# Kernel tuning notes

Hardware: AMD Instinct MI355X
Metric: run time of the kernel (lower is better)

The kernel has to match this reference:

```python
import jax, jax.numpy as jnp
import numpy as np
import math

B, D, L, H, K, CONV_N = 32, 128, 1024, 8, 7, 4
DK = D // H
EPS = 1e-5


def make_pos_encoding():
    i = np.arange(D, dtype=np.float64)
    freqs = np.where(i % 2 == 0, 10000.0 ** (-i / D), -(10000.0 ** ((1 - i) / D)))
    phases = np.where(i % 2 == 0, 0.0, math.pi / 2)
    pos = np.arange(L, dtype=np.float64)[None, :]  # [1, L]
    pe = np.sin(pos * freqs[:, None] + phases[:, None])  # [D, L]
    return jnp.asarray(pe, dtype=jnp.float32)


def layer_norm_2d(x, w, b):
    # nn.LayerNorm([D, L]) on [B, D, L]: normalize jointly over last two dims
    mu = jnp.mean(x, axis=(1, 2), keepdims=True)
    var = jnp.var(x, axis=(1, 2), keepdims=True)
    return (x - mu) * jax.lax.rsqrt(var + EPS) * w[None] + b[None]


def setup_inputs():
    key = jax.random.key(0)
    ks = jax.random.split(key, 24)
    s = 0.05
    x = jax.random.normal(ks[0], (B, D, L), jnp.float32)
    lengths = jax.random.randint(ks[1], (B,), L // 2, L + 1)
    mask = (jnp.arange(L)[None, :] >= lengths[:, None]).astype(jnp.float32)  # 1 = pad
    inp = {
        "x": x,
        "mask": mask,
        "pos_enc": make_pos_encoding(),
        "normb_w": jnp.ones((D, L), jnp.float32),
        "normb_b": jnp.zeros((D, L), jnp.float32),
        "dw_w": jax.random.normal(ks[2], (CONV_N, D, K), jnp.float32) * s,
        "dw_b": jnp.zeros((CONV_N, D), jnp.float32),
        "pw_w": jax.random.normal(ks[3], (CONV_N, D, D), jnp.float32) * s,
        "pw_b": jnp.zeros((CONV_N, D), jnp.float32),
        "norms_w": jnp.ones((CONV_N, D, L), jnp.float32),
        "norms_b": jnp.zeros((CONV_N, D, L), jnp.float32),
        "qw": jax.random.normal(ks[4], (D, D), jnp.float32) * s,
        "qb": jnp.zeros((D,), jnp.float32),
        "kw": jax.random.normal(ks[5], (D, D), jnp.float32) * s,
        "kb": jnp.zeros((D,), jnp.float32),
        "vw": jax.random.normal(ks[6], (D, D), jnp.float32) * s,
        "vb": jnp.zeros((D,), jnp.float32),
        "aw": jax.random.normal(ks[7], (D, D), jnp.float32) * s,  # attention output fc
        "ab": jnp.zeros((D,), jnp.float32),
        "norme_w": jnp.ones((D, L), jnp.float32),
        "norme_b": jnp.zeros((D, L), jnp.float32),
        "fw": jax.random.normal(ks[8], (D, D), jnp.float32) * s,  # final fc
        "fb": jnp.zeros((D,), jnp.float32),
    }
    return inp


def reference(x, mask, pos_enc, normb_w, normb_b, dw_w, dw_b, pw_w, pw_b,
              norms_w, norms_b, qw, qb, kw, kb, vw, vb, aw, ab,
              norme_w, norme_b, fw, fb):
    # positional encoding + pre-LN
    out = x + pos_enc[None]
    res = out
    out = layer_norm_2d(out, normb_w, normb_b)

    # conv stack (eval mode: dropout is identity)
    for i in range(CONV_N):
        h = jax.lax.conv_general_dilated(
            out, dw_w[i][:, None, :],  # depthwise: [D, 1, K]
            window_strides=(1,), padding=[(K // 2, K // 2)],
            dimension_numbers=("NCH", "OIH", "NCH"),
            feature_group_count=D) + dw_b[i][None, :, None]
        h = jnp.einsum("bcl,oc->bol", h, pw_w[i]) + pw_b[i][None, :, None]
        out = jax.nn.relu(h) + res
        res = out
        out = layer_norm_2d(out, norms_w[i], norms_b[i])

    # multi-head self-attention (manual bmm-softmax-bmm, scale 1/sqrt(d_k))
    xt = jnp.swapaxes(out, 1, 2)  # [B, L, D]
    q = (xt @ qw.T + qb).reshape(B, L, H, DK)
    k = (xt @ kw.T + kb).reshape(B, L, H, DK)
    v = (xt @ vw.T + vb).reshape(B, L, H, DK)
    scores = jnp.einsum("bqhd,bkhd->bhqk", q, k) * (1.0 / math.sqrt(DK))
    m = mask[:, None, None, :]  # broadcast over heads and query dim
    scores = scores * (1.0 - m) + m * (-1e30)
    attn = jax.nn.softmax(scores, axis=-1)
    o = jnp.einsum("bhqk,bkhd->bqhd", attn, v).reshape(B, L, D)
    o = o @ aw.T + ab
    o = jnp.swapaxes(o, 1, 2)  # [B, D, L]

    out = o + res
    res = out
    out = layer_norm_2d(out, norme_w, norme_b)
    out = jnp.einsum("bdl,ed->bel", out, fw) + fb[None, :, None]
    out = jax.nn.relu(out) + res
    return out
```

## Files before the change

### kernel.cpp

```cpp
#include <hip/hip_runtime.h>

#define NB 32
#define ND 128
#define NL 1024
#define NDL (ND*NL)
#define STATS_B 16
#define STATS_R (32*STATS_B)

typedef __attribute__((ext_vector_type(8))) short bf16x8;
typedef __attribute__((ext_vector_type(4))) float f32x4;
typedef unsigned short u16;

__device__ __forceinline__ f32x4 mfma_bf16_16x16x32(bf16x8 a, bf16x8 b, f32x4 c) {
#if defined(__HIP_DEVICE_COMPILE__)
  return __builtin_amdgcn_mfma_f32_16x16x32_bf16(a, b, c, 0, 0, 0);
#else
  return c;
#endif
}

__device__ __forceinline__ float exp2fast(float x) {
#if defined(__HIP_DEVICE_COMPILE__) && __has_builtin(__builtin_amdgcn_exp2f)
  return __builtin_amdgcn_exp2f(x);
#elif defined(__HIP_DEVICE_COMPILE__)
  return __expf(x * 0.6931471805599453f);
#else
  return x;
#endif
}

__device__ __forceinline__ float bf2f(u16 u) {
  union { unsigned u; float f; } c; c.u = ((unsigned)u) << 16; return c.f;
}
__device__ __forceinline__ u16 bf16rnd(float f) {
  union { float f; unsigned u; } c; c.f = f;
  return (u16)((c.u + 0x7FFFu + ((c.u >> 16) & 1u)) >> 16);
}
__device__ __forceinline__ unsigned packpair(float a, float b) {
  return (unsigned)bf16rnd(a) | ((unsigned)bf16rnd(b) << 16);
}
__device__ __forceinline__ unsigned packtrunc(float a, float b) {
  unsigned ua = __float_as_uint(a), ub = __float_as_uint(b);
  return (ub & 0xFFFF0000u) | (ua >> 16);
}
__device__ __forceinline__ bf16x8 packbf8(float4 a, float4 b) {
  union { unsigned u[4]; bf16x8 v; } r;
  r.u[0] = packpair(a.x, a.y); r.u[1] = packpair(a.z, a.w);
  r.u[2] = packpair(b.x, b.y); r.u[3] = packpair(b.z, b.w);
  return r.v;
}

__device__ __forceinline__ void blockRedAtomic(float s, float sq, float* base) {
  __shared__ float red[32];
#pragma unroll
  for (int off = 32; off > 0; off >>= 1) {
    s  += __shfl_down(s, off, 64);
    sq += __shfl_down(sq, off, 64);
  }
  int wave = threadIdx.x >> 6;
  int nw = blockDim.x >> 6;
  if ((threadIdx.x & 63) == 0) { red[wave*2] = s; red[wave*2+1] = sq; }
  __syncthreads();
  if (threadIdx.x == 0) {
    float ts = 0.f, tq = 0.f;
    for (int i = 0; i < nw; ++i) { ts += red[i*2]; tq += red[i*2+1]; }
    unsafeAtomicAdd(base,     ts);
    unsafeAtomicAdd(base + 1, tq);
  }
}

__global__ void k_zero(float* stats) {
  int t = threadIdx.x;
#pragma unroll
  for (int i = 0; i < 3; ++i) stats[i*1024 + t] = 0.f;
}

__global__ __launch_bounds__(256) void k_len(const float* __restrict__ mask,
                                             int* __restrict__ lenbuf) {
  __shared__ int csh;
  int b = blockIdx.x, tid = threadIdx.x;
  if (tid == 0) csh = 0;
  __syncthreads();
  int cnt = 0;
  for (int i = tid; i < NL; i += 256) cnt += (mask[(size_t)b*NL + i] == 0.f) ? 1 : 0;
#pragma unroll
  for (int off = 32; off > 0; off >>= 1) cnt += __shfl_down(cnt, off, 64);
  if ((tid & 63) == 0) atomicAdd(&csh, cnt);
  __syncthreads();
  if (tid == 0) lenbuf[b] = csh;
}

__global__ __launch_bounds__(256) void k_addpos(const float* __restrict__ x,
                                                const float* __restrict__ pe,
                                                u16* __restrict__ res,
                                                float* __restrict__ stats0) {
  int b = blockIdx.x >> 6;
  int off = ((blockIdx.x & 63) << 11) + (threadIdx.x << 3);
  const float4* xp = (const float4*)(x + (size_t)b*NDL + off);
  const float4* pp = (const float4*)(pe + off);
  float s = 0.f, sq = 0.f;
  float rv[8];
#pragma unroll
  for (int i = 0; i < 2; ++i) {
    float4 a = xp[i], p = pp[i];
    rv[i*4+0] = a.x + p.x; rv[i*4+1] = a.y + p.y;
    rv[i*4+2] = a.z + p.z; rv[i*4+3] = a.w + p.w;
  }
#pragma unroll
  for (int j = 0; j < 8; ++j) { s += rv[j]; sq += rv[j]*rv[j]; }
  uint4 pk;
  pk.x = packpair(rv[0], rv[1]); pk.y = packpair(rv[2], rv[3]);
  pk.z = packpair(rv[4], rv[5]); pk.w = packpair(rv[6], rv[7]);
  *(uint4*)(res + (size_t)b*NDL + off) = pk;
  blockRedAtomic(s, sq, stats0 + b*STATS_B);
}


__device__ __forceinline__ void load_w_frags16(const float* __restrict__ W,
                                               int wo, int lo, int hi, bf16x8 af[4]) {
#pragma unroll
  for (int kk = 0; kk < 4; ++kk) {
    const float4* wp = (const float4*)(W + (size_t)(wo + lo)*128 + kk*32 + hi*8);
    af[kk] = packbf8(wp[0], wp[1]);
  }
}

__device__ __forceinline__ void mfma_core16(const unsigned* xs, bf16x8 af[4],
                                            int lo, int hi, f32x4 acc[4]) {
#pragma unroll
  for (int ln = 0; ln < 4; ++ln) {
#pragma unroll
    for (int kk = 0; kk < 4; ++kk) {
      int l = ln*16 + lo;
      int off = (l*256 + kk*64 + hi*16) ^ ((lo & 7) << 4);
      bf16x8 bf = *(const bf16x8*)((const char*)xs + off);
      acc[ln] = mfma_bf16_16x16x32(af[kk], bf, acc[ln]);
    }
  }
}

__device__ __forceinline__ void conv_row8(const u16* __restrict__ srow,
                                          const float* __restrict__ lwrow,
                                          const float* __restrict__ lbrow,
                                          int base, float mu, float rstd,
                                          const float* wk, float bias0,
                                          float* h ) {
  float wa[14];
  bool interior = (base >= 4) && (base + 12 <= NL);
  if (interior) {
    const uint2* sp = (const uint2*)(srow + base - 4);
    const float4* wp = (const float4*)(lwrow + base - 4);
    const float4* bp = (const float4*)(lbrow + base - 4);
#pragma unroll
    for (int qd = 0; qd < 4; ++qd) {
      uint2 sv2 = sp[qd];
      float4 w4 = wp[qd], b4 = bp[qd];
      float sv[4] = {bf2f((u16)(sv2.x & 0xFFFF)), bf2f((u16)(sv2.x >> 16)),
                     bf2f((u16)(sv2.y & 0xFFFF)), bf2f((u16)(sv2.y >> 16))};
      float wv[4] = {w4.x, w4.y, w4.z, w4.w};
      float bv[4] = {b4.x, b4.y, b4.z, b4.w};
#pragma unroll
      for (int e = 0; e < 4; ++e) {
        int j = qd*4 + e - 1;
        if (j >= 0 && j < 14)
          wa[j] = (sv[e] - mu)*rstd*wv[e] + bv[e];
      }
    }
  } else {
#pragma unroll
    for (int j = 0; j < 14; ++j) {
      int gl = base + j - 3;
      float v = 0.f;
      if (gl >= 0 && gl < NL)
        v = (bf2f(srow[gl]) - mu)*rstd*lwrow[gl] + lbrow[gl];
      wa[j] = v;
    }
  }
#pragma unroll
  for (int l = 0; l < 8; ++l) {
    float acc = bias0;
#pragma unroll
    for (int j = 0; j < 7; ++j) acc += wa[l+j]*wk[j];
    h[l] = acc;
  }
}

template<int MODE>
__global__ __launch_bounds__(512) void k_gemm_mfma(
    const u16* __restrict__ src16, const float* __restrict__ W,
    const float* __restrict__ bias,
    const u16* __restrict__ res16, u16* __restrict__ wr16,
    float* __restrict__ outf,
    const float* __restrict__ lnw, const float* __restrict__ lnb,
    const float* __restrict__ dww, const float* __restrict__ dwb,
    const float* __restrict__ statsIn, float* __restrict__ statsOut) {
  __shared__ unsigned xs[4096];
  int b  = blockIdx.x >> 4;
  int l0 = (blockIdx.x & 15) << 6;
  int tid = threadIdx.x;
  int wave = tid >> 6, lane = tid & 63;
  int lo = lane & 15, hi = lane >> 4;
  int wo = wave * 16;

  float mu = 0.f, rstd = 0.f;
  if (MODE == 0 || MODE == 3) {
    mu = statsIn[b*STATS_B] * (1.f/NDL);
    rstd = rsqrtf(statsIn[b*STATS_B + 1]*(1.f/NDL) - mu*mu + 1e-5f);
  }

  if (MODE == 0) {
    int c2 = tid >> 3, lq = tid & 7;
    int c = c2*2, base = l0 + lq*8;
    float wk0[7], wk1[7];
#pragma unroll
    for (int j = 0; j < 7; ++j) { wk0[j] = dww[c*7 + j]; wk1[j] = dww[(c+1)*7 + j]; }
    const u16* sa = src16 + (size_t)b*NDL + (size_t)c*NL;
    const float* la  = lnw + (size_t)c*NL;
    const float* lbv = lnb + (size_t)c*NL;
    float h0[8], h1[8];
    conv_row8(sa,      la,      lbv,      base, mu, rstd, wk0, dwb[c],   h0);
    conv_row8(sa + NL, la + NL, lbv + NL, base, mu, rstd, wk1, dwb[c+1], h1);
#pragma unroll
    for (int l = 0; l < 8; ++l) {
      int ll = lq*8 + l;
      xs[(ll << 6) | (c2 ^ ((ll & 7) << 2))] = packpair(h0[l], h1[l]);
    }
  } else if (MODE == 1) {
    for (int i = tid; i < 1024; i += 512) {
      int c2 = i >> 4, lq = (i & 15) << 2;
      int c = c2*2;
      const u16* sp = src16 + (size_t)b*NDL + (size_t)c*NL + l0 + lq;
      uint2 ra = *(const uint2*)sp;
      uint2 rb = *(const uint2*)(sp + NL);
      unsigned wv[4];
      wv[0] = (ra.x & 0xFFFFu) | (rb.x << 16);
      wv[1] = (ra.x >> 16)     | (rb.x & 0xFFFF0000u);
      wv[2] = (ra.y & 0xFFFFu) | (rb.y << 16);
      wv[3] = (ra.y >> 16)     | (rb.y & 0xFFFF0000u);
#pragma unroll
      for (int j = 0; j < 4; ++j) {
        int l = lq + j;
        xs[(l << 6) | (c2 ^ ((l & 7) << 2))] = wv[j];
      }
    }
  } else {
    for (int i = tid; i < 1024; i += 512) {
      int c2 = i >> 4, lq = (i & 15) << 2;
      int c = c2*2;
      const u16* sp = src16 + (size_t)b*NDL + (size_t)c*NL + l0 + lq;
      uint2 ra = *(const uint2*)sp;
      uint2 rb = *(const uint2*)(sp + NL);
      float sa[4] = {bf2f((u16)(ra.x & 0xFFFF)), bf2f((u16)(ra.x >> 16)),
                     bf2f((u16)(ra.y & 0xFFFF)), bf2f((u16)(ra.y >> 16))};
      float sb[4] = {bf2f((u16)(rb.x & 0xFFFF)), bf2f((u16)(rb.x >> 16)),
                     bf2f((u16)(rb.y & 0xFFFF)), bf2f((u16)(rb.y >> 16))};
      size_t gi = (size_t)c*NL + l0 + lq;
      float4 w0 = *(const float4*)(lnw + gi), w1 = *(const float4*)(lnw + gi + NL);
      float4 bb0 = *(const float4*)(lnb + gi), bb1 = *(const float4*)(lnb + gi + NL);
      float va[4] = {(sa[0]-mu)*rstd*w0.x + bb0.x, (sa[1]-mu)*rstd*w0.y + bb0.y,
                     (sa[2]-mu)*rstd*w0.z + bb0.z, (sa[3]-mu)*rstd*w0.w + bb0.w};
      float vb[4] = {(sb[0]-mu)*rstd*w1.x + bb1.x, (sb[1]-mu)*rstd*w1.y + bb1.y,
                     (sb[2]-mu)*rstd*w1.z + bb1.z, (sb[3]-mu)*rstd*w1.w + bb1.w};
#pragma unroll
      for (int j = 0; j < 4; ++j) {
        int l = lq + j;
        xs[(l << 6) | (c2 ^ ((l & 7) << 2))] = packpair(va[j], vb[j]);
      }
    }
  }

  u16 rpre[16];
#pragma unroll
  for (int ln = 0; ln < 4; ++ln)
#pragma unroll
    for (int r = 0; r < 4; ++r)
      rpre[ln*4+r] = res16[((size_t)b*ND + wo + hi*4 + r)*NL + l0 + ln*16 + lo];

  bf16x8 af[4];
  load_w_frags16(W, wo, lo, hi, af);
  f32x4 acc[4];
#pragma unroll
  for (int ln = 0; ln < 4; ++ln) acc[ln] = (f32x4){0.f,0.f,0.f,0.f};

  __syncthreads();
  mfma_core16(xs, af, lo, hi, acc);

  if (MODE == 0 || MODE == 1) {
    float s = 0.f, sq = 0.f;
#pragma unroll
    for (int ln = 0; ln < 4; ++ln) {
      int l = l0 + ln*16 + lo;
#pragma unroll
      for (int r = 0; r < 4; ++r) {
        int o = wo + hi*4 + r;
        size_t gi = ((size_t)b*ND + o)*NL + l;
        float v = acc[ln][r] + bias[o];
        if (MODE == 0) v = fmaxf(v, 0.f);
        v += bf2f(rpre[ln*4+r]);
        wr16[gi] = bf16rnd(v);
        s += v; sq += v*v;
      }
    }
    blockRedAtomic(s, sq, statsOut + b*STATS_B);
  } else {
#pragma unroll
    for (int ln = 0; ln < 4; ++ln) {
      int l = l0 + ln*16 + lo;
#pragma unroll
      for (int r = 0; r < 4; ++r) {
        int o = wo + hi*4 + r;
        size_t gi = ((size_t)b*ND + o)*NL + l;
        outf[gi] = fmaxf(acc[ln][r] + bias[o], 0.f) + bf2f(rpre[ln*4+r]);
      }
    }
  }
}

__global__ __launch_bounds__(512) void k_qkv_mfma(
    const u16* __restrict__ src16,
    const float* __restrict__ qw, const float* __restrict__ kw, const float* __restrict__ vw,
    const float* __restrict__ qb, const float* __restrict__ kb, const float* __restrict__ vb,
    u16* __restrict__ qo, u16* __restrict__ ko, u16* __restrict__ vo,
    const float* __restrict__ lnw, const float* __restrict__ lnb,
    const float* __restrict__ statsIn) {
  __shared__ unsigned xs[4096];
  int b  = blockIdx.x >> 4;
  int l0 = (blockIdx.x & 15) << 6;
  int tid = threadIdx.x;
  int wave = tid >> 6, lane = tid & 63;
  int lo = lane & 15, hi = lane >> 4;
  int wo = wave * 16;

  float mu = statsIn[b*STATS_B] * (1.f/NDL);
  float rstd = rsqrtf(statsIn[b*STATS_B + 1]*(1.f/NDL) - mu*mu + 1e-5f);
  for (int i = tid; i < 1024; i += 512) {
    int c2 = i >> 4, lq = (i & 15) << 2;
    int c = c2*2;
    const u16* sp = src16 + (size_t)b*NDL + (size_t)c*NL + l0 + lq;
    uint2 ra = *(const uint2*)sp;
    uint2 rb = *(const uint2*)(sp + NL);
    float sa[4] = {bf2f((u16)(ra.x & 0xFFFF)), bf2f((u16)(ra.x >> 16)),
                   bf2f((u16)(ra.y & 0xFFFF)), bf2f((u16)(ra.y >> 16))};
    float sb[4] = {bf2f((u16)(rb.x & 0xFFFF)), bf2f((u16)(rb.x >> 16)),
                   bf2f((u16)(rb.y & 0xFFFF)), bf2f((u16)(rb.y >> 16))};
    size_t gi = (size_t)c*NL + l0 + lq;
    float4 w0 = *(const float4*)(lnw + gi), w1 = *(const float4*)(lnw + gi + NL);
    float4 bb0 = *(const float4*)(lnb + gi), bb1 = *(const float4*)(lnb + gi + NL);
    float va[4] = {(sa[0]-mu)*rstd*w0.x + bb0.x, (sa[1]-mu)*rstd*w0.y + bb0.y,
                   (sa[2]-mu)*rstd*w0.z + bb0.z, (sa[3]-mu)*rstd*w0.w + bb0.w};
    float vb4[4] = {(sb[0]-mu)*rstd*w1.x + bb1.x, (sb[1]-mu)*rstd*w1.y + bb1.y,
                    (sb[2]-mu)*rstd*w1.z + bb1.z, (sb[3]-mu)*rstd*w1.w + bb1.w};
#pragma unroll
    for (int j = 0; j < 4; ++j) {
      int l = lq + j;
      xs[(l << 6) | (c2 ^ ((l & 7) << 2))] = packpair(va[j], vb4[j]);
    }
  }
  __syncthreads();

  const float* Ws[3] = {qw, kw, vw};
  const float* Bs[3] = {qb, kb, vb};
  u16* Os[3] = {qo, ko, vo};
#pragma unroll 1
  for (int mat = 0; mat < 3; ++mat) {
    bf16x8 af[4];
    load_w_frags16(Ws[mat], wo, lo, hi, af);
    f32x4 acc[4];
#pragma unroll
    for (int ln = 0; ln < 4; ++ln) acc[ln] = (f32x4){0.f,0.f,0.f,0.f};
    mfma_core16(xs, af, lo, hi, acc);
    float oscale = (mat == 0) ? 0.25f*1.4426950408889634f : 1.0f;
    const float* bias = Bs[mat];
    u16* op = Os[mat];
#pragma unroll
    for (int ln = 0; ln < 4; ++ln) {
      int l = l0 + ln*16 + lo;
      int o4 = wo + hi*4;
      float vx = (acc[ln][0] + bias[o4+0]) * oscale;
      float vy = (acc[ln][1] + bias[o4+1]) * oscale;
      float vz = (acc[ln][2] + bias[o4+2]) * oscale;
      float vw4 = (acc[ln][3] + bias[o4+3]) * oscale;
      uint2 pk; pk.x = packpair(vx, vy); pk.y = packpair(vz, vw4);
      *(uint2*)(op + ((size_t)b*NL + l)*ND + o4) = pk;
    }
  }
}

template<bool MASKED>
__device__ __forceinline__ void attn_tile(bf16x8 kf0, bf16x8 kf1, bf16x8 vf,
                                          bf16x8 onesf, const bf16x8 qf[4],
                                          f32x4 acc[4], f32x4 dacc[4],
                                          int kb, int len, int hi) {
#pragma unroll
  for (int qt = 0; qt < 4; ++qt) {
    f32x4 z = (f32x4){0.f,0.f,0.f,0.f};
    f32x4 s0 = mfma_bf16_16x16x32(kf0, qf[qt], z);
    f32x4 s1 = mfma_bf16_16x16x32(kf1, qf[qt], z);
    float e[8];
#pragma unroll
    for (int r = 0; r < 4; ++r) {
      float e0 = exp2fast(s0[r]);
      float e1 = exp2fast(s1[r]);
      if (MASKED) {
        e0 = (kb + hi*4 + r < len)      ? e0 : 0.f;
        e1 = (kb + 16 + hi*4 + r < len) ? e1 : 0.f;
      }
      e[r] = e0; e[r+4] = e1;
    }
    union { unsigned u[4]; bf16x8 v; } pu;
    pu.u[0] = packtrunc(e[0], e[1]);
    pu.u[1] = packtrunc(e[2], e[3]);
    pu.u[2] = packtrunc(e[4], e[5]);
    pu.u[3] = packtrunc(e[6], e[7]);
    acc[qt]  = mfma_bf16_16x16x32(vf,    pu.v, acc[qt]);
    dacc[qt] = mfma_bf16_16x16x32(onesf, pu.v, dacc[qt]);
  }
}

__device__ __forceinline__ bf16x8 ldKrow(const u16* kbase, int key, int hi) {
  union { uint4 u; bf16x8 v; } r;
  r.u = *(const uint4*)(kbase + (size_t)key*ND + hi*8);
  return r.v;
}

__global__ __launch_bounds__(512) void k_attn_fused(
    const u16* __restrict__ q, const u16* __restrict__ k,
    const u16* __restrict__ v, const int* __restrict__ lenbuf,
    u16* __restrict__ att_t) {
  __shared__ short kv[16384];
  int bid = blockIdx.x;
  int b  = bid >> 4;
  int h  = (bid >> 1) & 7;
  int qh = bid & 1;
  int tid = threadIdx.x;
  int len = lenbuf[b];
  int nkt = (len + 31) >> 5;
  int kstage = nkt << 5;

  for (int idx = tid; idx < 2048; idx += 512) {
    int keyp = idx >> 2, vq = idx & 3;
    int key = keyp*2;
    if (key >= kstage) break;
    int vlo = vq*4;
    uint2 ra, rb; ra.x = ra.y = rb.x = rb.y = 0u;
    size_t voff = ((size_t)b*NL + key)*ND + h*16 + vlo;
    if (key < len)     ra = *(const uint2*)(v + voff);
    if (key + 1 < len) rb = *(const uint2*)(v + voff + ND);
    unsigned wv[4];
    wv[0] = (ra.x & 0xFFFFu) | (rb.x << 16);
    wv[1] = (ra.x >> 16)     | (rb.x & 0xFFFF0000u);
    wv[2] = (ra.y & 0xFFFFu) | (rb.y << 16);
    wv[3] = (ra.y >> 16)     | (rb.y & 0xFFFF0000u);
    int kt = key >> 5, w = key & 31;
    int vhi, ii;
    if (w < 16) { vhi = w >> 2; ii = w & 3; }
    else        { vhi = (w - 16) >> 2; ii = 4 + (w & 3); }
#pragma unroll
    for (int e = 0; e < 4; ++e)
      *(unsigned*)(kv + kt*512 + (vhi*16 + vlo + e)*8 + ii) = wv[e];
  }
  __syncthreads();

  int wave = tid >> 6, lane = tid & 63;
  int lo = lane & 15, hi = lane >> 4;
  int q0 = qh*512 + wave*64;

  bf16x8 qf[4];
#pragma unroll
  for (int qt = 0; qt < 4; ++qt) {
    if (hi < 2) {
      union { uint4 u; bf16x8 v; } qu;
      qu.u = *(const uint4*)(q + ((size_t)b*NL + q0 + qt*16 + lo)*ND + h*16 + hi*8);
      qf[qt] = qu.v;
    } else {
      qf[qt] = (bf16x8){0,0,0,0,0,0,0,0};
    }
  }
  const short oneb = (short)0x3F80;
  bf16x8 onesf = (bf16x8){oneb,oneb,oneb,oneb,oneb,oneb,oneb,oneb};
  f32x4 acc[4], dacc[4];
#pragma unroll
  for (int qt = 0; qt < 4; ++qt) {
    acc[qt]  = (f32x4){0.f,0.f,0.f,0.f};
    dacc[qt] = (f32x4){0.f,0.f,0.f,0.f};
  }

  int fullt = len >> 5;
  const u16* kbase = k + (size_t)b*NL*ND + h*16;

  bf16x8 cka = (bf16x8){0,0,0,0,0,0,0,0}, ckb = cka, cv;
  if (hi < 2) {
    cka = ldKrow(kbase, lo, hi);
    ckb = ldKrow(kbase, 16 + lo, hi);
  }
  cv = *(const bf16x8*)(kv + lane*8);

  for (int kt = 0; kt < nkt; ++kt) {
    bf16x8 nka = cka, nkb = ckb, nv = cv;
    if (kt + 1 < nkt) {
      int kb2 = (kt+1)*32;
      if (hi < 2) {
        nka = ldKrow(kbase, kb2 + lo, hi);
        nkb = ldKrow(kbase, kb2 + 16 + lo, hi);
      }
      nv = *(const bf16x8*)(kv + (kt+1)*512 + lane*8);
    }
    if (kt < fullt) attn_tile<false>(cka, ckb, cv, onesf, qf, acc, dacc, kt*32, len, hi);
    else            attn_tile<true >(cka, ckb, cv, onesf, qf, acc, dacc, kt*32, len, hi);
    cka = nka; ckb = nkb; cv = nv;
  }
#pragma unroll
  for (int qt = 0; qt < 4; ++qt) {
    float inv = 1.f / dacc[qt][0];
    size_t obase = ((size_t)b*ND + h*16)*NL + q0 + qt*16 + lo;
#pragma unroll
    for (int r = 0; r < 4; ++r)
      att_t[obase + (size_t)(hi*4 + r)*NL] = bf16rnd(acc[qt][r] * inv);
  }
}

extern "C" void kernel_launch(void* const* d_in, const int* in_sizes, int n_in,
                              void* d_out, int out_size, void* d_ws, size_t ws_size,
                              hipStream_t stream) {
  (void)in_sizes; (void)n_in; (void)out_size; (void)ws_size;
  const float* x       = (const float*)d_in[0];
  const float* mask    = (const float*)d_in[1];
  const float* pe      = (const float*)d_in[2];
  const float* normb_w = (const float*)d_in[3];
  const float* normb_b = (const float*)d_in[4];
  const float* dw_w    = (const float*)d_in[5];
  const float* dw_b    = (const float*)d_in[6];
  const float* pw_w    = (const float*)d_in[7];
  const float* pw_b    = (const float*)d_in[8];
  const float* norms_w = (const float*)d_in[9];
  const float* norms_b = (const float*)d_in[10];
  const float* qw      = (const float*)d_in[11];
  const float* qb      = (const float*)d_in[12];
  const float* kw      = (const float*)d_in[13];
  const float* kb      = (const float*)d_in[14];
  const float* vw      = (const float*)d_in[15];
  const float* vb      = (const float*)d_in[16];
  const float* aw      = (const float*)d_in[17];
  const float* ab      = (const float*)d_in[18];
  const float* norme_w = (const float*)d_in[19];
  const float* norme_b = (const float*)d_in[20];
  const float* fw      = (const float*)d_in[21];
  const float* fb      = (const float*)d_in[22];

  float* out = (float*)d_out;
  float* ws  = (float*)d_ws;
  const size_t NT = (size_t)NB*ND*NL;
  u16* resA = (u16*)ws;
  u16* resB = (u16*)(ws + NT/2);
  u16* qb16 = (u16*)(ws + NT);
  u16* kb16 = (u16*)(ws + 3*NT/2);
  u16* vb16 = (u16*)(ws + 2*NT);
  float* stats = ws + 3*NT;
  int* lenbuf = (int*)(stats + 6*STATS_R);
  u16* att16 = resB;

  k_zero<<<dim3(1), dim3(1024), 0, stream>>>(stats);
  k_len<<<dim3(NB), dim3(256), 0, stream>>>(mask, lenbuf);
  k_addpos<<<dim3(2048), dim3(256), 0, stream>>>(x, pe, resA, stats);

  for (int i = 0; i < 4; ++i) {
    const float* lw = (i == 0) ? normb_w : norms_w + (size_t)(i-1)*NDL;
    const float* lb = (i == 0) ? normb_b : norms_b + (size_t)(i-1)*NDL;
    const u16* rsrc = (i & 1) ? resB : resA;
    u16*       rdst = (i & 1) ? resA : resB;
    k_gemm_mfma<0><<<dim3(NB*16), dim3(512), 0, stream>>>(
        rsrc, pw_w + i*ND*ND, pw_b + i*ND, rsrc, rdst, nullptr,
        lw, lb, dw_w + i*ND*7, dw_b + i*ND,
        stats + i*STATS_R, stats + (i+1)*STATS_R);
  }

  const float* ln3w = norms_w + (size_t)3*NDL;
  const float* ln3b = norms_b + (size_t)3*NDL;
  k_qkv_mfma<<<dim3(NB*16), dim3(512), 0, stream>>>(
      resA, qw, kw, vw, qb, kb, vb, qb16, kb16, vb16, ln3w, ln3b, stats + 4*STATS_R);

  k_attn_fused<<<dim3(NB*8*2), dim3(512), 0, stream>>>(qb16, kb16, vb16, lenbuf, att16);

  k_gemm_mfma<1><<<dim3(NB*16), dim3(512), 0, stream>>>(
      att16, aw, ab, resA, resA, nullptr, nullptr, nullptr, nullptr, nullptr,
      nullptr, stats + 5*STATS_R);
  k_gemm_mfma<3><<<dim3(NB*16), dim3(512), 0, stream>>>(
      resA, fw, fb, resA, nullptr, out, norme_w, norme_b, nullptr, nullptr,
      stats + 5*STATS_R, nullptr);
}
```

Baseline: 172.1 us.

## Double threads per GEMM block and split attention queries across more blocks

The GEMM and QKV kernels now launch 1024 threads per block. Each wave covers 32 of the 64 L columns instead of all 64, and each thread does one staging chunk and a 4-wide conv instead of 8. The attention kernel now uses four query quarters per (batch, head) with 32 queries per wave, doubling the block count. The goal is more waves in flight to hide latency. The cost is that each block reloads K/V into shared memory twice as often, there are more atomics in the stats reductions, and register pressure is tighter under the new launch bounds.

```diff
diff --git a/kernel.cpp b/kernel.cpp
--- a/kernel.cpp
+++ b/kernel.cpp
@@ -125,13 +125,13 @@
   }
 }
 
-__device__ __forceinline__ void mfma_core16(const unsigned* xs, bf16x8 af[4],
-                                            int lo, int hi, f32x4 acc[4]) {
-#pragma unroll
-  for (int ln = 0; ln < 4; ++ln) {
+__device__ __forceinline__ void mfma_core2(const unsigned* xs, bf16x8 af[4],
+                                           int lo, int hi, int loff, f32x4 acc[2]) {
+#pragma unroll
+  for (int ln = 0; ln < 2; ++ln) {
 #pragma unroll
     for (int kk = 0; kk < 4; ++kk) {
-      int l = ln*16 + lo;
+      int l = loff + ln*16 + lo;
       int off = (l*256 + kk*64 + hi*16) ^ ((lo & 7) << 4);
       bf16x8 bf = *(const bf16x8*)((const char*)xs + off);
       acc[ln] = mfma_bf16_16x16x32(af[kk], bf, acc[ln]);
@@ -139,20 +139,20 @@
   }
 }
 
-__device__ __forceinline__ void conv_row8(const u16* __restrict__ srow,
+__device__ __forceinline__ void conv_row4(const u16* __restrict__ srow,
                                           const float* __restrict__ lwrow,
                                           const float* __restrict__ lbrow,
                                           int base, float mu, float rstd,
                                           const float* wk, float bias0,
                                           float* h ) {
-  float wa[14];
-  bool interior = (base >= 4) && (base + 12 <= NL);
+  float wa[10];
+  bool interior = (base >= 4) && (base + 8 <= NL);
   if (interior) {
     const uint2* sp = (const uint2*)(srow + base - 4);
     const float4* wp = (const float4*)(lwrow + base - 4);
     const float4* bp = (const float4*)(lbrow + base - 4);
 #pragma unroll
-    for (int qd = 0; qd < 4; ++qd) {
+    for (int qd = 0; qd < 3; ++qd) {
       uint2 sv2 = sp[qd];
       float4 w4 = wp[qd], b4 = bp[qd];
       float sv[4] = {bf2f((u16)(sv2.x & 0xFFFF)), bf2f((u16)(sv2.x >> 16)),
@@ -162,13 +162,13 @@
 #pragma unroll
       for (int e = 0; e < 4; ++e) {
         int j = qd*4 + e - 1;
-        if (j >= 0 && j < 14)
+        if (j >= 0 && j < 10)
           wa[j] = (sv[e] - mu)*rstd*wv[e] + bv[e];
       }
     }
   } else {
 #pragma unroll
-    for (int j = 0; j < 14; ++j) {
+    for (int j = 0; j < 10; ++j) {
       int gl = base + j - 3;
       float v = 0.f;
       if (gl >= 0 && gl < NL)
@@ -177,7 +177,7 @@
     }
   }
 #pragma unroll
-  for (int l = 0; l < 8; ++l) {
+  for (int l = 0; l < 4; ++l) {
     float acc = bias0;
 #pragma unroll
     for (int j = 0; j < 7; ++j) acc += wa[l+j]*wk[j];
@@ -186,7 +186,7 @@
 }
 
 template<int MODE>
-__global__ __launch_bounds__(512) void k_gemm_mfma(
+__global__ __launch_bounds__(1024, 8) void k_gemm_mfma(
     const u16* __restrict__ src16, const float* __restrict__ W,
     const float* __restrict__ bias,
     const u16* __restrict__ res16, u16* __restrict__ wr16,
@@ -200,7 +200,8 @@
   int tid = threadIdx.x;
   int wave = tid >> 6, lane = tid & 63;
   int lo = lane & 15, hi = lane >> 4;
-  int wo = wave * 16;
+  int wo = (wave & 7) * 16;
+  int loff = (wave >> 3) * 32;
 
   float mu = 0.f, rstd = 0.f;
   if (MODE == 0 || MODE == 3) {
@@ -208,88 +209,81 @@
     rstd = rsqrtf(statsIn[b*STATS_B + 1]*(1.f/NDL) - mu*mu + 1e-5f);
   }
 
+  int c2 = tid >> 4, lq4 = (tid & 15) << 2;
+  int c = c2*2;
   if (MODE == 0) {
-    int c2 = tid >> 3, lq = tid & 7;
-    int c = c2*2, base = l0 + lq*8;
+    int base = l0 + lq4;
     float wk0[7], wk1[7];
 #pragma unroll
     for (int j = 0; j < 7; ++j) { wk0[j] = dww[c*7 + j]; wk1[j] = dww[(c+1)*7 + j]; }
     const u16* sa = src16 + (size_t)b*NDL + (size_t)c*NL;
     const float* la  = lnw + (size_t)c*NL;
     const float* lbv = lnb + (size_t)c*NL;
-    float h0[8], h1[8];
-    conv_row8(sa,      la,      lbv,      base, mu, rstd, wk0, dwb[c],   h0);
-    conv_row8(sa + NL, la + NL, lbv + NL, base, mu, rstd, wk1, dwb[c+1], h1);
-#pragma unroll
-    for (int l = 0; l < 8; ++l) {
-      int ll = lq*8 + l;
+    float h0[4], h1[4];
+    conv_row4(sa,      la,      lbv,      base, mu, rstd, wk0, dwb[c],   h0);
+    conv_row4(sa + NL, la + NL, lbv + NL, base, mu, rstd, wk1, dwb[c+1], h1);
+#pragma unroll
+    for (int l = 0; l < 4; ++l) {
+      int ll = lq4 + l;
       xs[(ll << 6) | (c2 ^ ((ll & 7) << 2))] = packpair(h0[l], h1[l]);
     }
   } else if (MODE == 1) {
-    for (int i = tid; i < 1024; i += 512) {
-      int c2 = i >> 4, lq = (i & 15) << 2;
-      int c = c2*2;
-      const u16* sp = src16 + (size_t)b*NDL + (size_t)c*NL + l0 + lq;
-      uint2 ra = *(const uint2*)sp;
-      uint2 rb = *(const uint2*)(sp + NL);
-      unsigned wv[4];
-      wv[0] = (ra.x & 0xFFFFu) | (rb.x << 16);
-      wv[1] = (ra.x >> 16)     | (rb.x & 0xFFFF0000u);
-      wv[2] = (ra.y & 0xFFFFu) | (rb.y << 16);
-      wv[3] = (ra.y >> 16)     | (rb.y & 0xFFFF0000u);
-#pragma unroll
-      for (int j = 0; j < 4; ++j) {
-        int l = lq + j;
-        xs[(l << 6) | (c2 ^ ((l & 7) << 2))] = wv[j];
-      }
+    const u16* sp = src16 + (size_t)b*NDL + (size_t)c*NL + l0 + lq4;
+    uint2 ra = *(const uint2*)sp;
+    uint2 rb = *(const uint2*)(sp + NL);
+    unsigned wv[4];
+    wv[0] = (ra.x & 0xFFFFu) | (rb.x << 16);
+    wv[1] = (ra.x >> 16)     | (rb.x & 0xFFFF0000u);
+    wv[2] = (ra.y & 0xFFFFu) | (rb.y << 16);
+    wv[3] = (ra.y >> 16)     | (rb.y & 0xFFFF0000u);
+#pragma unroll
+    for (int j = 0; j < 4; ++j) {
+      int l = lq4 + j;
+      xs[(l << 6) | (c2 ^ ((l & 7) << 2))] = wv[j];
     }
   } else {
-    for (int i = tid; i < 1024; i += 512) {
-      int c2 = i >> 4, lq = (i & 15) << 2;
-      int c = c2*2;
-      const u16* sp = src16 + (size_t)b*NDL + (size_t)c*NL + l0 + lq;
-      uint2 ra = *(const uint2*)sp;
-      uint2 rb = *(const uint2*)(sp + NL);
-      float sa[4] = {bf2f((u16)(ra.x & 0xFFFF)), bf2f((u16)(ra.x >> 16)),
-                     bf2f((u16)(ra.y & 0xFFFF)), bf2f((u16)(ra.y >> 16))};
-      float sb[4] = {bf2f((u16)(rb.x & 0xFFFF)), bf2f((u16)(rb.x >> 16)),
-                     bf2f((u16)(rb.y & 0xFFFF)), bf2f((u16)(rb.y >> 16))};
-      size_t gi = (size_t)c*NL + l0 + lq;
-      float4 w0 = *(const float4*)(lnw + gi), w1 = *(const float4*)(lnw + gi + NL);
-      float4 bb0 = *(const float4*)(lnb + gi), bb1 = *(const float4*)(lnb + gi + NL);
-      float va[4] = {(sa[0]-mu)*rstd*w0.x + bb0.x, (sa[1]-mu)*rstd*w0.y + bb0.y,
-                     (sa[2]-mu)*rstd*w0.z + bb0.z, (sa[3]-mu)*rstd*w0.w + bb0.w};
-      float vb[4] = {(sb[0]-mu)*rstd*w1.x + bb1.x, (sb[1]-mu)*rstd*w1.y + bb1.y,
-                     (sb[2]-mu)*rstd*w1.z + bb1.z, (sb[3]-mu)*rstd*w1.w + bb1.w};
-#pragma unroll
-      for (int j = 0; j < 4; ++j) {
-        int l = lq + j;
-        xs[(l << 6) | (c2 ^ ((l & 7) << 2))] = packpair(va[j], vb[j]);
-      }
-    }
-  }
-
-  u16 rpre[16];
-#pragma unroll
-  for (int ln = 0; ln < 4; ++ln)
+    const u16* sp = src16 + (size_t)b*NDL + (size_t)c*NL + l0 + lq4;
+    uint2 ra = *(const uint2*)sp;
+    uint2 rb = *(const uint2*)(sp + NL);
+    float sa[4] = {bf2f((u16)(ra.x & 0xFFFF)), bf2f((u16)(ra.x >> 16)),
+                   bf2f((u16)(ra.y & 0xFFFF)), bf2f((u16)(ra.y >> 16))};
+    float sb[4] = {bf2f((u16)(rb.x & 0xFFFF)), bf2f((u16)(rb.x >> 16)),
+                   bf2f((u16)(rb.y & 0xFFFF)), bf2f((u16)(rb.y >> 16))};
+    size_t gi = (size_t)c*NL + l0 + lq4;
+    float4 w0 = *(const float4*)(lnw + gi), w1 = *(const float4*)(lnw + gi + NL);
+    float4 bb0 = *(const float4*)(lnb + gi), bb1 = *(const float4*)(lnb + gi + NL);
+    float va[4] = {(sa[0]-mu)*rstd*w0.x + bb0.x, (sa[1]-mu)*rstd*w0.y + bb0.y,
+                   (sa[2]-mu)*rstd*w0.z + bb0.z, (sa[3]-mu)*rstd*w0.w + bb0.w};
+    float vb[4] = {(sb[0]-mu)*rstd*w1.x + bb1.x, (sb[1]-mu)*rstd*w1.y + bb1.y,
+                   (sb[2]-mu)*rstd*w1.z + bb1.z, (sb[3]-mu)*rstd*w1.w + bb1.w};
+#pragma unroll
+    for (int j = 0; j < 4; ++j) {
+      int l = lq4 + j;
+      xs[(l << 6) | (c2 ^ ((l & 7) << 2))] = packpair(va[j], vb[j]);
+    }
+  }
+
+  u16 rpre[8];
+#pragma unroll
+  for (int ln = 0; ln < 2; ++ln)
 #pragma unroll
     for (int r = 0; r < 4; ++r)
-      rpre[ln*4+r] = res16[((size_t)b*ND + wo + hi*4 + r)*NL + l0 + ln*16 + lo];
+      rpre[ln*4+r] = res16[((size_t)b*ND + wo + hi*4 + r)*NL + l0 + loff + ln*16 + lo];
 
   bf16x8 af[4];
   load_w_frags16(W, wo, lo, hi, af);
-  f32x4 acc[4];
-#pragma unroll
-  for (int ln = 0; ln < 4; ++ln) acc[ln] = (f32x4){0.f,0.f,0.f,0.f};
+  f32x4 acc[2];
+#pragma unroll
+  for (int ln = 0; ln < 2; ++ln) acc[ln] = (f32x4){0.f,0.f,0.f,0.f};
 
   __syncthreads();
-  mfma_core16(xs, af, lo, hi, acc);
+  mfma_core2(xs, af, lo, hi, loff, acc);
 
   if (MODE == 0 || MODE == 1) {
     float s = 0.f, sq = 0.f;
 #pragma unroll
-    for (int ln = 0; ln < 4; ++ln) {
-      int l = l0 + ln*16 + lo;
+    for (int ln = 0; ln < 2; ++ln) {
+      int l = l0 + loff + ln*16 + lo;
 #pragma unroll
       for (int r = 0; r < 4; ++r) {
         int o = wo + hi*4 + r;
@@ -304,8 +298,8 @@
     blockRedAtomic(s, sq, statsOut + b*STATS_B);
   } else {
 #pragma unroll
-    for (int ln = 0; ln < 4; ++ln) {
-      int l = l0 + ln*16 + lo;
+    for (int ln = 0; ln < 2; ++ln) {
+      int l = l0 + loff + ln*16 + lo;
 #pragma unroll
       for (int r = 0; r < 4; ++r) {
         int o = wo + hi*4 + r;
@@ -316,7 +310,7 @@
   }
 }
 
-__global__ __launch_bounds__(512) void k_qkv_mfma(
+__global__ __launch_bounds__(1024, 8) void k_qkv_mfma(
     const u16* __restrict__ src16,
     const float* __restrict__ qw, const float* __restrict__ kw, const float* __restrict__ vw,
     const float* __restrict__ qb, const float* __restrict__ kb, const float* __restrict__ vb,
@@ -329,21 +323,22 @@
   int tid = threadIdx.x;
   int wave = tid >> 6, lane = tid & 63;
   int lo = lane & 15, hi = lane >> 4;
-  int wo = wave * 16;
+  int wo = (wave & 7) * 16;
+  int loff = (wave >> 3) * 32;
 
   float mu = statsIn[b*STATS_B] * (1.f/NDL);
   float rstd = rsqrtf(statsIn[b*STATS_B + 1]*(1.f/NDL) - mu*mu + 1e-5f);
-  for (int i = tid; i < 1024; i += 512) {
-    int c2 = i >> 4, lq = (i & 15) << 2;
+  {
+    int c2 = tid >> 4, lq4 = (tid & 15) << 2;
     int c = c2*2;
-    const u16* sp = src16 + (size_t)b*NDL + (size_t)c*NL + l0 + lq;
+    const u16* sp = src16 + (size_t)b*NDL + (size_t)c*NL + l0 + lq4;
     uint2 ra = *(const uint2*)sp;
     uint2 rb = *(const uint2*)(sp + NL);
     float sa[4] = {bf2f((u16)(ra.x & 0xFFFF)), bf2f((u16)(ra.x >> 16)),
                    bf2f((u16)(ra.y & 0xFFFF)), bf2f((u16)(ra.y >> 16))};
     float sb[4] = {bf2f((u16)(rb.x & 0xFFFF)), bf2f((u16)(rb.x >> 16)),
                    bf2f((u16)(rb.y & 0xFFFF)), bf2f((u16)(rb.y >> 16))};
-    size_t gi = (size_t)c*NL + l0 + lq;
+    size_t gi = (size_t)c*NL + l0 + lq4;
     float4 w0 = *(const float4*)(lnw + gi), w1 = *(const float4*)(lnw + gi + NL);
     float4 bb0 = *(const float4*)(lnb + gi), bb1 = *(const float4*)(lnb + gi + NL);
     float va[4] = {(sa[0]-mu)*rstd*w0.x + bb0.x, (sa[1]-mu)*rstd*w0.y + bb0.y,
@@ -352,7 +347,7 @@
                     (sb[2]-mu)*rstd*w1.z + bb1.z, (sb[3]-mu)*rstd*w1.w + bb1.w};
 #pragma unroll
     for (int j = 0; j < 4; ++j) {
-      int l = lq + j;
+      int l = lq4 + j;
       xs[(l << 6) | (c2 ^ ((l & 7) << 2))] = packpair(va[j], vb4[j]);
     }
   }
@@ -365,16 +360,16 @@
   for (int mat = 0; mat < 3; ++mat) {
     bf16x8 af[4];
     load_w_frags16(Ws[mat], wo, lo, hi, af);
-    f32x4 acc[4];
-#pragma unroll
-    for (int ln = 0; ln < 4; ++ln) acc[ln] = (f32x4){0.f,0.f,0.f,0.f};
-    mfma_core16(xs, af, lo, hi, acc);
+    f32x4 acc[2];
+#pragma unroll
+    for (int ln = 0; ln < 2; ++ln) acc[ln] = (f32x4){0.f,0.f,0.f,0.f};
+    mfma_core2(xs, af, lo, hi, loff, acc);
     float oscale = (mat == 0) ? 0.25f*1.4426950408889634f : 1.0f;
     const float* bias = Bs[mat];
     u16* op = Os[mat];
 #pragma unroll
-    for (int ln = 0; ln < 4; ++ln) {
-      int l = l0 + ln*16 + lo;
+    for (int ln = 0; ln < 2; ++ln) {
+      int l = l0 + loff + ln*16 + lo;
       int o4 = wo + hi*4;
       float vx = (acc[ln][0] + bias[o4+0]) * oscale;
       float vy = (acc[ln][1] + bias[o4+1]) * oscale;
@@ -388,11 +383,11 @@
 
 template<bool MASKED>
 __device__ __forceinline__ void attn_tile(bf16x8 kf0, bf16x8 kf1, bf16x8 vf,
-                                          bf16x8 onesf, const bf16x8 qf[4],
-                                          f32x4 acc[4], f32x4 dacc[4],
+                                          bf16x8 onesf, const bf16x8 qf[2],
+                                          f32x4 acc[2], f32x4 dacc[2],
                                           int kb, int len, int hi) {
 #pragma unroll
-  for (int qt = 0; qt < 4; ++qt) {
+  for (int qt = 0; qt < 2; ++qt) {
     f32x4 z = (f32x4){0.f,0.f,0.f,0.f};
     f32x4 s0 = mfma_bf16_16x16x32(kf0, qf[qt], z);
     f32x4 s1 = mfma_bf16_16x16x32(kf1, qf[qt], z);
@@ -423,15 +418,15 @@
   return r.v;
 }
 
-__global__ __launch_bounds__(512) void k_attn_fused(
+__global__ __launch_bounds__(512, 8) void k_attn_fused(
     const u16* __restrict__ q, const u16* __restrict__ k,
     const u16* __restrict__ v, const int* __restrict__ lenbuf,
     u16* __restrict__ att_t) {
   __shared__ short kv[16384];
   int bid = blockIdx.x;
-  int b  = bid >> 4;
-  int h  = (bid >> 1) & 7;
-  int qh = bid & 1;
+  int b  = bid >> 5;
+  int h  = (bid >> 2) & 7;
+  int qq = bid & 3;
   int tid = threadIdx.x;
   int len = lenbuf[b];
   int nkt = (len + 31) >> 5;
@@ -463,11 +458,11 @@
 
   int wave = tid >> 6, lane = tid & 63;
   int lo = lane & 15, hi = lane >> 4;
-  int q0 = qh*512 + wave*64;
-
-  bf16x8 qf[4];
-#pragma unroll
-  for (int qt = 0; qt < 4; ++qt) {
+  int q0 = qq*256 + wave*32;
+
+  bf16x8 qf[2];
+#pragma unroll
+  for (int qt = 0; qt < 2; ++qt) {
     if (hi < 2) {
       union { uint4 u; bf16x8 v; } qu;
       qu.u = *(const uint4*)(q + ((size_t)b*NL + q0 + qt*16 + lo)*ND + h*16 + hi*8);
@@ -478,9 +473,9 @@
   }
   const short oneb = (short)0x3F80;
   bf16x8 onesf = (bf16x8){oneb,oneb,oneb,oneb,oneb,oneb,oneb,oneb};
-  f32x4 acc[4], dacc[4];
-#pragma unroll
-  for (int qt = 0; qt < 4; ++qt) {
+  f32x4 acc[2], dacc[2];
+#pragma unroll
+  for (int qt = 0; qt < 2; ++qt) {
     acc[qt]  = (f32x4){0.f,0.f,0.f,0.f};
     dacc[qt] = (f32x4){0.f,0.f,0.f,0.f};
   }
@@ -510,7 +505,7 @@
     cka = nka; ckb = nkb; cv = nv;
   }
 #pragma unroll
-  for (int qt = 0; qt < 4; ++qt) {
+  for (int qt = 0; qt < 2; ++qt) {
     float inv = 1.f / dacc[qt][0];
     size_t obase = ((size_t)b*ND + h*16)*NL + q0 + qt*16 + lo;
 #pragma unroll
@@ -568,7 +563,7 @@
     const float* lb = (i == 0) ? normb_b : norms_b + (size_t)(i-1)*NDL;
     const u16* rsrc = (i & 1) ? resB : resA;
     u16*       rdst = (i & 1) ? resA : resB;
-    k_gemm_mfma<0><<<dim3(NB*16), dim3(512), 0, stream>>>(
+    k_gemm_mfma<0><<<dim3(NB*16), dim3(1024), 0, stream>>>(
         rsrc, pw_w + i*ND*ND, pw_b + i*ND, rsrc, rdst, nullptr,
         lw, lb, dw_w + i*ND*7, dw_b + i*ND,
         stats + i*STATS_R, stats + (i+1)*STATS_R);
@@ -576,15 +571,15 @@
 
   const float* ln3w = norms_w + (size_t)3*NDL;
   const float* ln3b = norms_b + (size_t)3*NDL;
-  k_qkv_mfma<<<dim3(NB*16), dim3(512), 0, stream>>>(
+  k_qkv_mfma<<<dim3(NB*16), dim3(1024), 0, stream>>>(
       resA, qw, kw, vw, qb, kb, vb, qb16, kb16, vb16, ln3w, ln3b, stats + 4*STATS_R);
 
-  k_attn_fused<<<dim3(NB*8*2), dim3(512), 0, stream>>>(qb16, kb16, vb16, lenbuf, att16);
-
-  k_gemm_mfma<1><<<dim3(NB*16), dim3(512), 0, stream>>>(
+  k_attn_fused<<<dim3(NB*8*4), dim3(512), 0, stream>>>(qb16, kb16, vb16, lenbuf, att16);
+
+  k_gemm_mfma<1><<<dim3(NB*16), dim3(1024), 0, stream>>>(
       att16, aw, ab, resA, resA, nullptr, nullptr, nullptr, nullptr, nullptr,
       nullptr, stats + 5*STATS_R);
-  k_gemm_mfma<3><<<dim3(NB*16), dim3(512), 0, stream>>>(
+  k_gemm_mfma<3><<<dim3(NB*16), dim3(1024), 0, stream>>>(
       resA, fw, fb, resA, nullptr, out, norme_w, norme_b, nullptr, nullptr,
       stats + 5*STATS_R, nullptr);
 }
```

New measurement: 272.6 us. +58.4%, slower.
